# Optimization experiments

Measured on AMD Instinct MI355X. Metric: run time of the kernel, lower is better.

## Reference

```python
import jax, jax.numpy as jnp
import numpy as np

N = 50000
E = 800000
D = 128
EPS = 1e-12


def setup_inputs() -> dict:
    key = jax.random.key(0)
    ks = jax.random.split(key, 16)
    s = 1.0 / np.sqrt(D)
    inp = {
        "x": jax.random.normal(ks[0], (N, D), dtype=jnp.float32),
        "edge_src": jax.random.randint(ks[1], (E,), 0, N, dtype=jnp.int32),
        "edge_dst": jax.random.randint(ks[2], (E,), 0, N, dtype=jnp.int32),
    }
    names = ["Wpool0", "Wself0", "Wneigh0", "Wpool1", "Wself1", "Wneigh1"]
    for i, n in enumerate(names):
        inp[n] = jax.random.uniform(ks[3 + i], (D, D), dtype=jnp.float32, minval=-s, maxval=s)
    for i, n in enumerate(["bpool0", "b0", "bpool1", "b1"]):
        inp[n] = jax.random.uniform(ks[9 + i], (D,), dtype=jnp.float32, minval=-s, maxval=s)
    return inp


def _sage_pool(h, src, dst, Wpool, bpool, Wself, Wneigh, b):
    # per-neighbor transform: relu(fc_pool(h_src))
    m = jax.nn.relu(h @ Wpool.T + bpool)            # [N, D]
    # gather -> segment max over destination nodes (irregular access)
    agg = jax.ops.segment_max(m[src], dst, num_segments=N)  # [N, D], -inf for empty
    deg = jax.ops.segment_sum(jnp.ones((E,), jnp.float32), dst, num_segments=N)
    h_neigh = jnp.where(deg[:, None] > 0, agg, 0.0)  # DGL: zero for isolated nodes
    return h @ Wself.T + h_neigh @ Wneigh.T + b


def _l2norm(h):
    # torch F.normalize(dim=1, eps=1e-12)
    n = jnp.sqrt(jnp.sum(h * h, axis=1, keepdims=True))
    return h / jnp.maximum(n, EPS)


def reference(x, edge_src, edge_dst,
              Wpool0, Wself0, Wneigh0, Wpool1, Wself1, Wneigh1,
              bpool0, b0, bpool1, b1):
    # layer 0 (not last): conv -> relu -> normalize -> dropout(p=0)
    h = _sage_pool(x, edge_src, edge_dst, Wpool0, bpool0, Wself0, Wneigh0, b0)
    h = jax.nn.relu(h)
    h = _l2norm(h)
    enc_feat_input = h  # l == n_layers - 2
    # layer 1 (last): conv only
    h = _sage_pool(h, edge_src, edge_dst, Wpool1, bpool1, Wself1, Wneigh1, b1)
    return h, enc_feat_input
```

## Files before the change

### kernel.cpp

```cpp
#include <hip/hip_runtime.h>
#include <hip/hip_fp16.h>

#define DD 128
#define BK_SHIFT 6
#define BK_NODES 64
#define NBLK 256
#define SCAN_T 1024
#define SCAN_E 8
#define SCAN_CHUNK (SCAN_T * SCAN_E)

typedef __attribute__((ext_vector_type(8))) _Float16 f16x8;
typedef __attribute__((ext_vector_type(4))) float f32x4;

__global__ void prep_w(const float* __restrict__ W0, const float* __restrict__ W1,
                       const float* __restrict__ W2, const float* __restrict__ W3,
                       const float* __restrict__ W4, const float* __restrict__ W5,
                       __half* __restrict__ Wh) {
    int idx = blockIdx.x * 256 + threadIdx.x;
    int wi = idx >> 14;
    int off = idx & 16383;
    int j = off >> 7;
    int k = off & 127;
    float a;
    switch (wi) {
        case 0: a = W0[off]; break;
        case 1: a = W1[off]; break;
        case 2: a = W2[off]; break;
        case 3: a = W3[off]; break;
        case 4: a = W4[off]; break;
        default: a = W5[off]; break;
    }
    int k2 = k ^ ((j & 7) << 3);
    Wh[(size_t)wi * 16384 + j * DD + k2] = __float2half(a);
}

__global__ __launch_bounds__(256) void hist2d_kernel(const int* __restrict__ dst,
                                                     int* __restrict__ hist2d,
                                                     int E, int NB, int chunk) {
    extern __shared__ int h[];
    int t = threadIdx.x, b = blockIdx.x;
    for (int i = t; i < NB; i += 256) h[i] = 0;
    __syncthreads();
    int e0 = b * chunk, e1 = min(e0 + chunk, E);
    for (int e = e0 + t; e < e1; e += 256)
        atomicAdd(&h[dst[e] >> BK_SHIFT], 1);
    __syncthreads();
    for (int i = t; i < NB; i += 256) hist2d[i * NBLK + b] = h[i];
}

__global__ __launch_bounds__(SCAN_T) void partial_reduce(const int* __restrict__ data,
                                                         int* __restrict__ bsum, int n) {
    __shared__ int s[SCAN_T];
    int t = threadIdx.x;
    int i0 = blockIdx.x * SCAN_CHUNK + t * SCAN_E;
    int sum = 0;
#pragma unroll
    for (int u = 0; u < SCAN_E; ++u) {
        int i = i0 + u;
        sum += (i < n) ? data[i] : 0;
    }
    s[t] = sum;
    __syncthreads();
    for (int off = SCAN_T / 2; off > 0; off >>= 1) {
        if (t < off) s[t] += s[t + off];
        __syncthreads();
    }
    if (t == 0) bsum[blockIdx.x] = s[0];
}

__global__ __launch_bounds__(SCAN_T) void scan_excl_inplace(int* __restrict__ data,
                                                            const int* __restrict__ bsum, int n) {
    __shared__ int s[SCAN_T];
    int t = threadIdx.x;
    int b = blockIdx.x;
    int carry = 0;
    for (int k = 0; k < b; ++k) carry += bsum[k];
    int i0 = b * SCAN_CHUNK + t * SCAN_E;
    int v[SCAN_E];
    int sum = 0;
#pragma unroll
    for (int u = 0; u < SCAN_E; ++u) {
        v[u] = (i0 + u < n) ? data[i0 + u] : 0;
        sum += v[u];
    }
    s[t] = sum;
    __syncthreads();
    for (int off = 1; off < SCAN_T; off <<= 1) {
        int x = (t >= off) ? s[t - off] : 0;
        __syncthreads();
        s[t] += x;
        __syncthreads();
    }
    int run = s[t] - sum + carry;
#pragma unroll
    for (int u = 0; u < SCAN_E; ++u) {
        int i = i0 + u;
        if (i < n) {
            data[i] = run;
            run += v[u];
        }
    }
}

__global__ __launch_bounds__(256) void bin_edges2(const int* __restrict__ src,
                                                  const int* __restrict__ dst,
                                                  const int* __restrict__ base,
                                                  unsigned* __restrict__ ebuf,
                                                  int E, int NB, int chunk) {
    extern __shared__ int h[];
    int t = threadIdx.x, b = blockIdx.x;
    for (int i = t; i < NB; i += 256) h[i] = base[i * NBLK + b];
    __syncthreads();
    int e0 = b * chunk, e1 = min(e0 + chunk, E);
    for (int e = e0 + t; e < e1; e += 256) {
        int d = dst[e];
        int p = atomicAdd(&h[d >> BK_SHIFT], 1);
        ebuf[p] = ((unsigned)src[e] << BK_SHIFT) | (unsigned)(d & (BK_NODES - 1));
    }
}

__global__ __launch_bounds__(256) void build_csr(const unsigned* __restrict__ ebuf,
                                                 const int* __restrict__ base,
                                                 int* __restrict__ rowptr,
                                                 int* __restrict__ csr_src, int N, int NB, int E) {
    __shared__ int cnt[BK_NODES];
    __shared__ int cur[BK_NODES];
    int b = blockIdx.x;
    int t = threadIdx.x;
    int beg = base[b * NBLK];
    int end = (b == NB - 1) ? E : base[(b + 1) * NBLK];
    if (b == 0 && t == 0) rowptr[0] = 0;
    if (t < BK_NODES) cnt[t] = 0;
    __syncthreads();
    for (int e = beg + t; e < end; e += 256)
        atomicAdd(&cnt[ebuf[e] & (BK_NODES - 1)], 1);
    __syncthreads();
    if (t < 64) {
        int v = cnt[t];
        int inc = v;
#pragma unroll
        for (int off = 1; off < 64; off <<= 1) {
            int x = __shfl_up(inc, off);
            if (t >= off) inc += x;
        }
        cur[t] = beg + inc - v;
        int node = b * BK_NODES + t;
        if (node < N) rowptr[node + 1] = beg + inc;
    }
    __syncthreads();
    for (int e = beg + t; e < end; e += 256) {
        unsigned v = ebuf[e];
        int p = atomicAdd(&cur[v & (BK_NODES - 1)], 1);
        csr_src[p] = (int)(v >> BK_SHIFT);
    }
}

__global__ __launch_bounds__(256) void segmax_half(const __half* __restrict__ m,
                                                   const int* __restrict__ rowptr,
                                                   const int* __restrict__ csr_src,
                                                   __half* __restrict__ agg, int n) {
    int node = blockIdx.x * 4 + (threadIdx.x >> 6);
    if (node >= n) return;
    int lane = threadIdx.x & 63;
    int beg = rowptr[node], end = rowptr[node + 1];
    const __half* mp = m + lane * 2;
    float2 mx[8];
#pragma unroll
    for (int u = 0; u < 8; ++u) mx[u] = make_float2(0.f, 0.f);
    int e = beg;
    for (; e + 8 <= end; e += 8) {
#pragma unroll
        for (int u = 0; u < 8; ++u) {
            int s = csr_src[e + u];
            float2 v = __half22float2(*(const __half2*)(mp + (size_t)s * DD));
            mx[u].x = fmaxf(mx[u].x, v.x);
            mx[u].y = fmaxf(mx[u].y, v.y);
        }
    }
    for (; e < end; ++e) {
        int s = csr_src[e];
        float2 v = __half22float2(*(const __half2*)(mp + (size_t)s * DD));
        mx[0].x = fmaxf(mx[0].x, v.x);
        mx[0].y = fmaxf(mx[0].y, v.y);
    }
#pragma unroll
    for (int u = 4; u > 0; u >>= 1)
#pragma unroll
        for (int k = 0; k < u; ++k) {
            mx[k].x = fmaxf(mx[k].x, mx[k + u].x);
            mx[k].y = fmaxf(mx[k].y, mx[k + u].y);
        }
    *(__half2*)(agg + (size_t)node * DD + lane * 2) = __float22half2_rn(mx[0]);
}

template <int EPI, bool FUSED>
__global__ __launch_bounds__(256) void gemm_f16(
    const float* __restrict__ A,
    const __half* __restrict__ WA,
    const __half* __restrict__ G,
    const __half* __restrict__ WG,
    const float* __restrict__ bias,
    float* __restrict__ outf, __half* __restrict__ outh, int nrows) {
    __shared__ __half Ws[DD * DD];
    int tid = threadIdx.x;
    int lane = tid & 63;
    int w = tid >> 6;
    int l16 = lane & 15;
    int lg = lane >> 4;
    int rbase = blockIdx.x * 128 + w * 32;

    {
        const f32x4* src = (const f32x4*)(const void*)WA;
        f32x4* dst = (f32x4*)(void*)Ws;
#pragma unroll
        for (int i = 0; i < 8; ++i) dst[i * 256 + tid] = src[i * 256 + tid];
    }
    __syncthreads();

    int ar0 = min(rbase + l16, nrows - 1);
    int ar1 = min(rbase + 16 + l16, nrows - 1);
    size_t aoff0 = (size_t)ar0 * DD;
    size_t aoff1 = (size_t)ar1 * DD;

    f32x4 acc[2][8];
#pragma unroll
    for (int mt = 0; mt < 2; ++mt)
#pragma unroll
        for (int nt = 0; nt < 8; ++nt) acc[mt][nt] = (f32x4){0.f, 0.f, 0.f, 0.f};

    int swz = (l16 & 7) << 3;

#pragma unroll
    for (int kk = 0; kk < 4; ++kk) {
        int k0 = kk * 32 + lg * 8;
        f16x8 a0, a1;
        {
            float4 u0 = *(const float4*)(A + aoff0 + k0);
            float4 u1 = *(const float4*)(A + aoff0 + k0 + 4);
            a0[0] = (_Float16)u0.x; a0[1] = (_Float16)u0.y;
            a0[2] = (_Float16)u0.z; a0[3] = (_Float16)u0.w;
            a0[4] = (_Float16)u1.x; a0[5] = (_Float16)u1.y;
            a0[6] = (_Float16)u1.z; a0[7] = (_Float16)u1.w;
            u0 = *(const float4*)(A + aoff1 + k0);
            u1 = *(const float4*)(A + aoff1 + k0 + 4);
            a1[0] = (_Float16)u0.x; a1[1] = (_Float16)u0.y;
            a1[2] = (_Float16)u0.z; a1[3] = (_Float16)u0.w;
            a1[4] = (_Float16)u1.x; a1[5] = (_Float16)u1.y;
            a1[6] = (_Float16)u1.z; a1[7] = (_Float16)u1.w;
        }
        int klds = k0 ^ swz;
#pragma unroll
        for (int nt = 0; nt < 8; ++nt) {
            f16x8 wh = *(const f16x8*)(const void*)(Ws + (nt * 16 + l16) * DD + klds);
            acc[0][nt] = __builtin_amdgcn_mfma_f32_16x16x32_f16(a0, wh, acc[0][nt], 0, 0, 0);
            acc[1][nt] = __builtin_amdgcn_mfma_f32_16x16x32_f16(a1, wh, acc[1][nt], 0, 0, 0);
        }
    }

    if constexpr (FUSED) {
        __syncthreads();
        {
            const f32x4* src = (const f32x4*)(const void*)WG;
            f32x4* dst = (f32x4*)(void*)Ws;
#pragma unroll
            for (int i = 0; i < 8; ++i) dst[i * 256 + tid] = src[i * 256 + tid];
        }
        __syncthreads();
#pragma unroll
        for (int kk = 0; kk < 4; ++kk) {
            int k0 = kk * 32 + lg * 8;
            f16x8 g0 = *(const f16x8*)(const void*)(G + aoff0 + k0);
            f16x8 g1 = *(const f16x8*)(const void*)(G + aoff1 + k0);
            int klds = k0 ^ swz;
#pragma unroll
            for (int nt = 0; nt < 8; ++nt) {
                f16x8 uh = *(const f16x8*)(const void*)(Ws + (nt * 16 + l16) * DD + klds);
                acc[0][nt] = __builtin_amdgcn_mfma_f32_16x16x32_f16(g0, uh, acc[0][nt], 0, 0, 0);
                acc[1][nt] = __builtin_amdgcn_mfma_f32_16x16x32_f16(g1, uh, acc[1][nt], 0, 0, 0);
            }
        }
    }

    float bv[8];
#pragma unroll
    for (int nt = 0; nt < 8; ++nt) bv[nt] = bias[nt * 16 + l16];

#pragma unroll
    for (int mt = 0; mt < 2; ++mt) {
#pragma unroll
        for (int r = 0; r < 4; ++r) {
            int row = rbase + mt * 16 + lg * 4 + r;
            float vv[8];
            float s = 0.f;
#pragma unroll
            for (int nt = 0; nt < 8; ++nt) {
                float v = acc[mt][nt][r] + bv[nt];
                if (EPI >= 1) v = fmaxf(v, 0.f);
                vv[nt] = v;
                s += v * v;
            }
            if constexpr (EPI == 2) {
                s += __shfl_xor(s, 1);
                s += __shfl_xor(s, 2);
                s += __shfl_xor(s, 4);
                s += __shfl_xor(s, 8);
                float sc = 1.0f / fmaxf(sqrtf(s), 1e-12f);
#pragma unroll
                for (int nt = 0; nt < 8; ++nt) vv[nt] *= sc;
            }
            if (row < nrows) {
                if constexpr (EPI == 1) {
#pragma unroll
                    for (int nt = 0; nt < 8; ++nt)
                        outh[(size_t)row * DD + nt * 16 + l16] = __float2half(vv[nt]);
                } else {
#pragma unroll
                    for (int nt = 0; nt < 8; ++nt)
                        outf[(size_t)row * DD + nt * 16 + l16] = vv[nt];
                }
            }
        }
    }
}

static inline size_t align16(size_t x) { return (x + 15) & ~(size_t)15; }

extern "C" void kernel_launch(void* const* d_in, const int* in_sizes, int n_in,
                              void* d_out, int out_size, void* d_ws, size_t ws_size,
                              hipStream_t stream) {
    const float* x  = (const float*)d_in[0];
    const int* esrc = (const int*)d_in[1];
    const int* edst = (const int*)d_in[2];
    const float* Wm[6];
    for (int i = 0; i < 6; ++i) Wm[i] = (const float*)d_in[3 + i];
    const float* bpool0 = (const float*)d_in[9];
    const float* b0     = (const float*)d_in[10];
    const float* bpool1 = (const float*)d_in[11];
    const float* b1     = (const float*)d_in[12];

    int N = in_sizes[0] / DD;
    int E = in_sizes[1];
    int NB = (N + BK_NODES - 1) >> BK_SHIFT;
    int chunk = (E + NBLK - 1) / NBLK;
    int nh = NB * NBLK;
    int nscan = (nh + SCAN_CHUNK - 1) / SCAN_CHUNK;

    char* p = (char*)d_ws;
    __half* Wh     = (__half*)p;   p += align16((size_t)6 * 16384 * 2);
    __half* m      = (__half*)p;   p += align16((size_t)N * DD * 2);
    __half* agg    = (__half*)p;   p += align16((size_t)N * DD * 2);
    int* hist2d    = (int*)p;      p += align16((size_t)nh * 4);
    int* bsum      = (int*)p;      p += align16((size_t)nscan * 4);
    int* rowptr    = (int*)p;      p += align16((size_t)(N + 1) * 4);
    unsigned* ebuf = (unsigned*)p; p += align16((size_t)E * 4);
    int* csr_src   = (int*)p;      p += align16((size_t)E * 4);

    float* out_h   = (float*)d_out;
    float* out_enc = (float*)d_out + (size_t)N * DD;

    prep_w<<<384, 256, 0, stream>>>(Wm[0], Wm[1], Wm[2], Wm[3], Wm[4], Wm[5], Wh);
    hist2d_kernel<<<NBLK, 256, NB * 4, stream>>>(edst, hist2d, E, NB, chunk);
    partial_reduce<<<nscan, SCAN_T, 0, stream>>>(hist2d, bsum, nh);
    scan_excl_inplace<<<nscan, SCAN_T, 0, stream>>>(hist2d, bsum, nh);
    bin_edges2<<<NBLK, 256, NB * 4, stream>>>(esrc, edst, hist2d, ebuf, E, NB, chunk);
    build_csr<<<NB, 256, 0, stream>>>(ebuf, hist2d, rowptr, csr_src, N, NB, E);

    int gb = (N + 127) / 128;
    int sb = (N + 3) / 4;

    gemm_f16<1, false><<<gb, 256, 0, stream>>>(x, Wh + 0 * 16384, nullptr, nullptr,
                                               bpool0, nullptr, m, N);
    segmax_half<<<sb, 256, 0, stream>>>(m, rowptr, csr_src, agg, N);
    gemm_f16<2, true><<<gb, 256, 0, stream>>>(x, Wh + 1 * 16384, agg, Wh + 2 * 16384,
                                              b0, out_enc, nullptr, N);

    gemm_f16<1, false><<<gb, 256, 0, stream>>>(out_enc, Wh + 3 * 16384, nullptr, nullptr,
                                               bpool1, nullptr, m, N);
    segmax_half<<<sb, 256, 0, stream>>>(m, rowptr, csr_src, agg, N);
    gemm_f16<0, true><<<gb, 256, 0, stream>>>(out_enc, Wh + 4 * 16384, agg, Wh + 5 * 16384,
                                              b1, out_h, nullptr, N);
}
```

Baseline: 178.3 us.

## Store GEMM inputs as fp16 and widen segment-max gathers to 16-byte loads

Adds a kernel that converts x to fp16 once, and has the layer-0 output GEMM also write an fp16 copy of the normalized features. All GEMMs then read fp16 A operands directly instead of loading fp32 and converting, which halves A-side traffic. The segment-max kernel is rewritten so each wave handles four edges at once, with 16 lanes each doing 16-byte f16x8 loads. Results are combined with packed fp16 max and cross-lane shuffles. The cost is an extra conversion pass over x, an extra fp16 store of the encoder output, and a larger workspace.

```diff
diff --git a/kernel.cpp b/kernel.cpp
--- a/kernel.cpp
+++ b/kernel.cpp
@@ -11,6 +11,14 @@
 
 typedef __attribute__((ext_vector_type(8))) _Float16 f16x8;
 typedef __attribute__((ext_vector_type(4))) float f32x4;
+
+union h8u { f16x8 v; int i[4]; };
+
+static __device__ __forceinline__ f16x8 vmax8(f16x8 a, f16x8 b) {
+#pragma unroll
+    for (int i = 0; i < 8; ++i) a[i] = a[i] > b[i] ? a[i] : b[i];
+    return a;
+}
 
 __global__ void prep_w(const float* __restrict__ W0, const float* __restrict__ W1,
                        const float* __restrict__ W2, const float* __restrict__ W3,
@@ -34,6 +42,17 @@
     Wh[(size_t)wi * 16384 + j * DD + k2] = __float2half(a);
 }
 
+__global__ void prep_x(const float* __restrict__ x, __half* __restrict__ xh, int n8) {
+    int i = blockIdx.x * 256 + threadIdx.x;
+    if (i >= n8) return;
+    float4 u0 = *(const float4*)(x + (size_t)i * 8);
+    float4 u1 = *(const float4*)(x + (size_t)i * 8 + 4);
+    f16x8 v;
+    v[0] = (_Float16)u0.x; v[1] = (_Float16)u0.y; v[2] = (_Float16)u0.z; v[3] = (_Float16)u0.w;
+    v[4] = (_Float16)u1.x; v[5] = (_Float16)u1.y; v[6] = (_Float16)u1.z; v[7] = (_Float16)u1.w;
+    *(f16x8*)(xh + (size_t)i * 8) = v;
+}
+
 __global__ __launch_bounds__(256) void hist2d_kernel(const int* __restrict__ dst,
                                                      int* __restrict__ hist2d,
                                                      int E, int NB, int chunk) {
@@ -155,47 +174,57 @@
     }
 }
 
-__global__ __launch_bounds__(256) void segmax_half(const __half* __restrict__ m,
-                                                   const int* __restrict__ rowptr,
-                                                   const int* __restrict__ csr_src,
-                                                   __half* __restrict__ agg, int n) {
+__global__ __launch_bounds__(256) void segmax2(const __half* __restrict__ m,
+                                               const int* __restrict__ rowptr,
+                                               const int* __restrict__ csr_src,
+                                               __half* __restrict__ agg, int n) {
     int node = blockIdx.x * 4 + (threadIdx.x >> 6);
     if (node >= n) return;
     int lane = threadIdx.x & 63;
+    int g = lane >> 4;
+    int l = lane & 15;
     int beg = rowptr[node], end = rowptr[node + 1];
-    const __half* mp = m + lane * 2;
-    float2 mx[8];
-#pragma unroll
-    for (int u = 0; u < 8; ++u) mx[u] = make_float2(0.f, 0.f);
-    int e = beg;
-    for (; e + 8 <= end; e += 8) {
-#pragma unroll
-        for (int u = 0; u < 8; ++u) {
-            int s = csr_src[e + u];
-            float2 v = __half22float2(*(const __half2*)(mp + (size_t)s * DD));
-            mx[u].x = fmaxf(mx[u].x, v.x);
-            mx[u].y = fmaxf(mx[u].y, v.y);
-        }
-    }
-    for (; e < end; ++e) {
-        int s = csr_src[e];
-        float2 v = __half22float2(*(const __half2*)(mp + (size_t)s * DD));
-        mx[0].x = fmaxf(mx[0].x, v.x);
-        mx[0].y = fmaxf(mx[0].y, v.y);
-    }
-#pragma unroll
-    for (int u = 4; u > 0; u >>= 1)
-#pragma unroll
-        for (int k = 0; k < u; ++k) {
-            mx[k].x = fmaxf(mx[k].x, mx[k + u].x);
-            mx[k].y = fmaxf(mx[k].y, mx[k + u].y);
-        }
-    *(__half2*)(agg + (size_t)node * DD + lane * 2) = __float22half2_rn(mx[0]);
+    const __half* mp = m + l * 8;
+
+    f16x8 acc0 = (f16x8)0, acc1 = (f16x8)0, acc2 = (f16x8)0, acc3 = (f16x8)0;
+
+    int e = beg + g;
+    for (; e + 12 < end; e += 16) {
+        int s0 = csr_src[e];
+        int s1 = csr_src[e + 4];
+        int s2 = csr_src[e + 8];
+        int s3 = csr_src[e + 12];
+        f16x8 u0 = *(const f16x8*)(mp + (size_t)s0 * DD);
+        f16x8 u1 = *(const f16x8*)(mp + (size_t)s1 * DD);
+        f16x8 u2 = *(const f16x8*)(mp + (size_t)s2 * DD);
+        f16x8 u3 = *(const f16x8*)(mp + (size_t)s3 * DD);
+        acc0 = vmax8(acc0, u0);
+        acc1 = vmax8(acc1, u1);
+        acc2 = vmax8(acc2, u2);
+        acc3 = vmax8(acc3, u3);
+    }
+    for (; e < end; e += 4) {
+        int s0 = csr_src[e];
+        f16x8 u0 = *(const f16x8*)(mp + (size_t)s0 * DD);
+        acc0 = vmax8(acc0, u0);
+    }
+
+    h8u a;
+    a.v = vmax8(vmax8(acc0, acc1), vmax8(acc2, acc3));
+#pragma unroll
+    for (int off = 16; off <= 32; off <<= 1) {
+        h8u b;
+#pragma unroll
+        for (int c = 0; c < 4; ++c) b.i[c] = __shfl_xor(a.i[c], off);
+        a.v = vmax8(a.v, b.v);
+    }
+    if (g == 0)
+        *(f16x8*)(agg + (size_t)node * DD + l * 8) = a.v;
 }
 
 template <int EPI, bool FUSED>
 __global__ __launch_bounds__(256) void gemm_f16(
-    const float* __restrict__ A,
+    const __half* __restrict__ A,
     const __half* __restrict__ WA,
     const __half* __restrict__ G,
     const __half* __restrict__ WG,
@@ -233,21 +262,8 @@
 #pragma unroll
     for (int kk = 0; kk < 4; ++kk) {
         int k0 = kk * 32 + lg * 8;
-        f16x8 a0, a1;
-        {
-            float4 u0 = *(const float4*)(A + aoff0 + k0);
-            float4 u1 = *(const float4*)(A + aoff0 + k0 + 4);
-            a0[0] = (_Float16)u0.x; a0[1] = (_Float16)u0.y;
-            a0[2] = (_Float16)u0.z; a0[3] = (_Float16)u0.w;
-            a0[4] = (_Float16)u1.x; a0[5] = (_Float16)u1.y;
-            a0[6] = (_Float16)u1.z; a0[7] = (_Float16)u1.w;
-            u0 = *(const float4*)(A + aoff1 + k0);
-            u1 = *(const float4*)(A + aoff1 + k0 + 4);
-            a1[0] = (_Float16)u0.x; a1[1] = (_Float16)u0.y;
-            a1[2] = (_Float16)u0.z; a1[3] = (_Float16)u0.w;
-            a1[4] = (_Float16)u1.x; a1[5] = (_Float16)u1.y;
-            a1[6] = (_Float16)u1.z; a1[7] = (_Float16)u1.w;
-        }
+        f16x8 a0 = *(const f16x8*)(const void*)(A + aoff0 + k0);
+        f16x8 a1 = *(const f16x8*)(const void*)(A + aoff1 + k0);
         int klds = k0 ^ swz;
 #pragma unroll
         for (int nt = 0; nt < 8; ++nt) {
@@ -317,6 +333,11 @@
 #pragma unroll
                     for (int nt = 0; nt < 8; ++nt)
                         outf[(size_t)row * DD + nt * 16 + l16] = vv[nt];
+                    if (EPI == 2 && outh != nullptr) {
+#pragma unroll
+                        for (int nt = 0; nt < 8; ++nt)
+                            outh[(size_t)row * DD + nt * 16 + l16] = __float2half(vv[nt]);
+                    }
                 }
             }
         }
@@ -347,6 +368,8 @@
 
     char* p = (char*)d_ws;
     __half* Wh     = (__half*)p;   p += align16((size_t)6 * 16384 * 2);
+    __half* xh     = (__half*)p;   p += align16((size_t)N * DD * 2);
+    __half* ench   = (__half*)p;   p += align16((size_t)N * DD * 2);
     __half* m      = (__half*)p;   p += align16((size_t)N * DD * 2);
     __half* agg    = (__half*)p;   p += align16((size_t)N * DD * 2);
     int* hist2d    = (int*)p;      p += align16((size_t)nh * 4);
@@ -359,6 +382,7 @@
     float* out_enc = (float*)d_out + (size_t)N * DD;
 
     prep_w<<<384, 256, 0, stream>>>(Wm[0], Wm[1], Wm[2], Wm[3], Wm[4], Wm[5], Wh);
+    prep_x<<<(N * DD / 8 + 255) / 256, 256, 0, stream>>>(x, xh, N * DD / 8);
     hist2d_kernel<<<NBLK, 256, NB * 4, stream>>>(edst, hist2d, E, NB, chunk);
     partial_reduce<<<nscan, SCAN_T, 0, stream>>>(hist2d, bsum, nh);
     scan_excl_inplace<<<nscan, SCAN_T, 0, stream>>>(hist2d, bsum, nh);
@@ -368,15 +392,15 @@
     int gb = (N + 127) / 128;
     int sb = (N + 3) / 4;
 
-    gemm_f16<1, false><<<gb, 256, 0, stream>>>(x, Wh + 0 * 16384, nullptr, nullptr,
+    gemm_f16<1, false><<<gb, 256, 0, stream>>>(xh, Wh + 0 * 16384, nullptr, nullptr,
                                                bpool0, nullptr, m, N);
-    segmax_half<<<sb, 256, 0, stream>>>(m, rowptr, csr_src, agg, N);
-    gemm_f16<2, true><<<gb, 256, 0, stream>>>(x, Wh + 1 * 16384, agg, Wh + 2 * 16384,
-                                              b0, out_enc, nullptr, N);
-
-    gemm_f16<1, false><<<gb, 256, 0, stream>>>(out_enc, Wh + 3 * 16384, nullptr, nullptr,
+    segmax2<<<sb, 256, 0, stream>>>(m, rowptr, csr_src, agg, N);
+    gemm_f16<2, true><<<gb, 256, 0, stream>>>(xh, Wh + 1 * 16384, agg, Wh + 2 * 16384,
+                                              b0, out_enc, ench, N);
+
+    gemm_f16<1, false><<<gb, 256, 0, stream>>>(ench, Wh + 3 * 16384, nullptr, nullptr,
                                                bpool1, nullptr, m, N);
-    segmax_half<<<sb, 256, 0, stream>>>(m, rowptr, csr_src, agg, N);
-    gemm_f16<0, true><<<gb, 256, 0, stream>>>(out_enc, Wh + 4 * 16384, agg, Wh + 5 * 16384,
+    segmax2<<<sb, 256, 0, stream>>>(m, rowptr, csr_src, agg, N);
+    gemm_f16<0, true><<<gb, 256, 0, stream>>>(ench, Wh + 4 * 16384, agg, Wh + 5 * 16384,
                                               b1, out_h, nullptr, N);
 }
```

New measurement: 173.6 us. -2.6%, faster.
